# Optimization experiments

Measured on AMD Instinct MI355X. Metric: run time of the kernel, lower is better.

The kernel has to match this reference:

```python
import jax, jax.numpy as jnp
import numpy as np

B, T, I, H, L, O = 64, 1024, 256, 512, 2, 256


def setup_inputs() -> dict:
    key = jax.random.key(0)
    ks = jax.random.split(key, 12)
    s = 1.0 / np.sqrt(H)  # PyTorch RNN init scale
    return {
        "x": jax.random.normal(ks[0], (B, T, I), jnp.float32),
        "W_ih0": jax.random.normal(ks[1], (3 * H, I), jnp.float32) * s,
        "W_hh0": jax.random.normal(ks[2], (3 * H, H), jnp.float32) * s,
        "b_ih0": jax.random.normal(ks[3], (3 * H,), jnp.float32) * s,
        "b_hh0": jax.random.normal(ks[4], (3 * H,), jnp.float32) * s,
        "W_ih1": jax.random.normal(ks[5], (3 * H, H), jnp.float32) * s,
        "W_hh1": jax.random.normal(ks[6], (3 * H, H), jnp.float32) * s,
        "b_ih1": jax.random.normal(ks[7], (3 * H,), jnp.float32) * s,
        "b_hh1": jax.random.normal(ks[8], (3 * H,), jnp.float32) * s,
        "fc_w": jax.random.normal(ks[9], (O, H), jnp.float32) * s,
        "fc_b": jax.random.normal(ks[10], (O,), jnp.float32) * s,
    }


def gru_layer(x, W_ih, W_hh, b_ih, b_hh):
    """One PyTorch-convention GRU layer, batch_first input [B,T,*], h0=0."""
    Bt, Tt, _ = x.shape
    Hh = W_hh.shape[1]
    # Precompute input-side gate pre-activations for all timesteps: [T,B,3H]
    xg = (jnp.einsum('bti,gi->btg', x, W_ih) + b_ih).transpose(1, 0, 2)

    def step(h, xg_t):
        hg = h @ W_hh.T + b_hh                      # [B,3H]
        xr, xz, xn = jnp.split(xg_t, 3, axis=-1)
        hr, hz, hn = jnp.split(hg, 3, axis=-1)
        r = jax.nn.sigmoid(xr + hr)
        z = jax.nn.sigmoid(xz + hz)
        n = jnp.tanh(xn + r * hn)
        h_new = (1.0 - z) * n + z * h
        return h_new, h_new

    h0 = jnp.zeros((Bt, Hh), x.dtype)
    hT, hs = jax.lax.scan(step, h0, xg)
    return hs.transpose(1, 0, 2), hT  # [B,T,H], [B,H]


def reference(x, W_ih0, W_hh0, b_ih0, b_hh0, W_ih1, W_hh1, b_ih1, b_hh1, fc_w, fc_b):
    out0, h0 = gru_layer(x, W_ih0, W_hh0, b_ih0, b_hh0)
    out1, h1 = gru_layer(out0, W_ih1, W_hh1, b_ih1, b_hh1)
    hidden = jnp.stack([h0, h1], axis=0)            # [num_layers, B, H]
    flat = out1.reshape(-1, out1.shape[-1])          # [B*T, H]
    out = flat @ fc_w.T + fc_b                       # [B*T, O]
    return out, hidden
```

## Files before the change

kernel.cpp:

```cpp
#include <hip/hip_runtime.h>
#include <hip/hip_bf16.h>
#include <hip/hip_fp16.h>
#include <stdint.h>
#include <type_traits>

#define B_ 64
#define T_ 1024
#define I_ 256
#define H_ 512
#define G3_ 1536
#define O_ 256

typedef __attribute__((ext_vector_type(4))) float floatx4;
typedef __attribute__((ext_vector_type(8))) short short8;
typedef __attribute__((ext_vector_type(2))) _Float16 half2v;
typedef __attribute__((ext_vector_type(4))) unsigned int u32x4;

#define BARX() __asm__ volatile("s_waitcnt lgkmcnt(0)\n\ts_barrier" ::: "memory")

static __device__ __forceinline__ float fdot2f(uint32_t a, uint32_t b, float c) {
#if __has_builtin(__builtin_amdgcn_fdot2)
  return __builtin_amdgcn_fdot2(__builtin_bit_cast(half2v, a),
                                __builtin_bit_cast(half2v, b), c, false);
#else
  __half2 ha = __builtin_bit_cast(__half2, a);
  __half2 hb = __builtin_bit_cast(__half2, b);
  float2 fa = __half22float2(ha), fb = __half22float2(hb);
  return c + fa.x * fb.x + fa.y * fb.y;
#endif
}

static __device__ __forceinline__ float sigmoid_f(float x) {
  float e = __expf(-fabsf(x));
  float a = 1.f / (1.f + e);
  return x >= 0.f ? a : 1.f - a;
}
static __device__ __forceinline__ float tanh_f(float x) {
  float e = __expf(-2.f * fabsf(x));
  float a = (1.f - e) / (1.f + e);
  return x >= 0.f ? a : -a;
}
static __device__ __forceinline__ uint32_t pack_h2(float a, float b) {
  return (uint32_t)__half_as_ushort(__float2half(a)) |
         ((uint32_t)__half_as_ushort(__float2half(b)) << 16);
}
static __device__ __forceinline__ uint32_t pack_bf2(float a, float b) {
  return (uint32_t)__builtin_bit_cast(unsigned short, __float2bfloat16(a)) |
         ((uint32_t)__builtin_bit_cast(unsigned short, __float2bfloat16(b)) << 16);
}

__global__ void init_kernel(const float* __restrict__ Whh0, const float* __restrict__ Whh1,
                            const float* __restrict__ bih0, const float* __restrict__ bhh0,
                            const float* __restrict__ bih1, const float* __restrict__ bhh1,
                            uint32_t* __restrict__ wpack, float* __restrict__ biasv,
                            uint32_t* __restrict__ hstate) {
  int idx = blockIdx.x * 256 + threadIdx.x;
  if (idx < 786432) {
    int l = idx / 393216, rem = idx % 393216;
    int rc = rem / 49152;
    int rem2 = rem % 49152;
    int s = rem2 / 6144;
    int rem3 = rem2 % 6144;
    int j = rem3 / 96;
    int i = rem3 % 96;
    int g = i >> 5, pp = i & 31;
    const float* W = l ? Whh1 : Whh0;
    int row = g * 512 + rc * 64 + j;
    int k = s * 64 + pp * 2;
    uint32_t lo = __half_as_ushort(__float2half(W[(size_t)row * 512 + k]));
    uint32_t hi = __half_as_ushort(__float2half(W[(size_t)row * 512 + k + 1]));
    wpack[idx] = lo | (hi << 16);
  }
  int i2 = idx - 786432;
  if (i2 >= 0 && i2 < 3072) {
    int l = i2 / 1536, n = i2 % 1536;
    const float* bi = l ? bih1 : bih0;
    const float* bh = l ? bhh1 : bhh0;
    biasv[i2] = bi[n] + (n < 1024 ? bh[n] : 0.f);
  }
  int i3 = idx - (786432 + 3072);
  if (i3 >= 0 && i3 < 32768) hstate[i3] = 0u;
}

template <typename TA, typename TC>
__global__ __launch_bounds__(256, 2) void gemm_bt(
    const TA* __restrict__ A, const float* __restrict__ Bw,
    const float* __restrict__ bias, TC* __restrict__ C,
    int K, int lda, int ldc, int tcshift, int t0, int Ttot) {
  __shared__ unsigned short As[128 * 40];
  __shared__ unsigned short Bs[128 * 40];
  const int tid = threadIdx.x;
  const int bm = blockIdx.x, bn = blockIdx.y;
  const int r = tid >> 1, hf = tid & 1;

  const int m = bm * 128 + r;
  const long arow = (long)(m >> tcshift) * Ttot + t0 + (m & ((1 << tcshift) - 1));
  const TA* ap = A + arow * (long)lda + hf * 16;
  const int n = bn * 128 + r;
  const float* bp = Bw + (long)n * K + hf * 16;

  const int wid = tid >> 6, lane = tid & 63;
  const int wm = (wid >> 1) * 64, wn = (wid & 1) * 64;
  const int m16 = lane & 15, quad = lane >> 4;

  floatx4 acc[4][4];
#pragma unroll
  for (int i = 0; i < 4; ++i)
#pragma unroll
    for (int j = 0; j < 4; ++j) acc[i][j] = 0.f;

  for (int k0 = 0; k0 < K; k0 += 32) {
    unsigned short ta[16], tb[16];
    if constexpr (std::is_same<TA, float>::value) {
      const float4* p = (const float4*)(ap + k0);
#pragma unroll
      for (int q = 0; q < 4; ++q) {
        float4 v = p[q];
        ta[q * 4 + 0] = __builtin_bit_cast(unsigned short, __float2bfloat16(v.x));
        ta[q * 4 + 1] = __builtin_bit_cast(unsigned short, __float2bfloat16(v.y));
        ta[q * 4 + 2] = __builtin_bit_cast(unsigned short, __float2bfloat16(v.z));
        ta[q * 4 + 3] = __builtin_bit_cast(unsigned short, __float2bfloat16(v.w));
      }
    } else {
      const uint4* p = (const uint4*)(ap + k0);
      *(uint4*)&ta[0] = p[0];
      *(uint4*)&ta[8] = p[1];
    }
    {
      const float4* p = (const float4*)(bp + k0);
#pragma unroll
      for (int q = 0; q < 4; ++q) {
        float4 v = p[q];
        tb[q * 4 + 0] = __builtin_bit_cast(unsigned short, __float2bfloat16(v.x));
        tb[q * 4 + 1] = __builtin_bit_cast(unsigned short, __float2bfloat16(v.y));
        tb[q * 4 + 2] = __builtin_bit_cast(unsigned short, __float2bfloat16(v.z));
        tb[q * 4 + 3] = __builtin_bit_cast(unsigned short, __float2bfloat16(v.w));
      }
    }
    *(uint4*)&As[r * 40 + hf * 16] = *(uint4*)&ta[0];
    *(uint4*)&As[r * 40 + hf * 16 + 8] = *(uint4*)&ta[8];
    *(uint4*)&Bs[r * 40 + hf * 16] = *(uint4*)&tb[0];
    *(uint4*)&Bs[r * 40 + hf * 16 + 8] = *(uint4*)&tb[8];
    __syncthreads();
    short8 af[4], bfr[4];
#pragma unroll
    for (int mt = 0; mt < 4; ++mt)
      af[mt] = *(const short8*)&As[(wm + mt * 16 + m16) * 40 + quad * 8];
#pragma unroll
    for (int nt = 0; nt < 4; ++nt)
      bfr[nt] = *(const short8*)&Bs[(wn + nt * 16 + m16) * 40 + quad * 8];
#pragma unroll
    for (int mt = 0; mt < 4; ++mt)
#pragma unroll
      for (int nt = 0; nt < 4; ++nt)
        acc[mt][nt] = __builtin_amdgcn_mfma_f32_16x16x32_bf16(af[mt], bfr[nt],
                                                              acc[mt][nt], 0, 0, 0);
    __syncthreads();
  }
#pragma unroll
  for (int mt = 0; mt < 4; ++mt)
#pragma unroll
    for (int nt = 0; nt < 4; ++nt)
#pragma unroll
      for (int rr = 0; rr < 4; ++rr) {
        int grow = bm * 128 + wm + mt * 16 + quad * 4 + rr;
        int gcol = bn * 128 + wn + nt * 16 + m16;
        float v = acc[mt][nt][rr];
        if (bias) v += bias[gcol];
        if constexpr (std::is_same<TC, float>::value)
          C[(long)grow * ldc + gcol] = v;
        else
          C[(long)grow * ldc + gcol] = __float2half(v);
      }
}

__global__ __launch_bounds__(512, 1) void gru_rec(
    const uint32_t* __restrict__ wpack, const uint32_t* __restrict__ xgd,
    const float* __restrict__ bhh, uint32_t* __restrict__ hstate,
    uint32_t* __restrict__ outw, uint64_t* __restrict__ pkts,
    float* __restrict__ hid_out,
    int t0, int Tc, int outT, int outT0, int last) {
  const int tid = threadIdx.x;
  const int s = tid >> 6;
  const int j = tid & 63;
  const int bp = blockIdx.x & 31;
  const int rc = blockIdx.x >> 5;
  const int b2 = j >> 5;
  const int m = j & 31;
  const int bgat = 2 * bp + b2;

  __shared__ uint32_t hb[2][8][32];
  __shared__ float part[2][2][3][8][64];

  u32x4 W[24];
  {
    const uint32_t* wb = wpack + (((size_t)rc * 8 + s) * 64 + j) * 96;
#pragma unroll
    for (int q = 0; q < 24; ++q)
      asm volatile("global_load_dwordx4 %0, %1, off"
                   : "=v"(W[q])
                   : "v"(wb + q * 4));
    asm volatile("s_waitcnt vmcnt(0)" ::: "memory");
  }

  float hold0 = 0.f, hold1 = 0.f, bn0 = 0.f, bn1 = 0.f;
  uint32_t xrw = 0, xzw = 0, xnw = 0;
  if (s == 0) {
    uint32_t hv = hstate[bgat * 256 + rc * 32 + m];
    __half2 hh = __builtin_bit_cast(__half2, hv);
    hold0 = __half2float(hh.x);
    hold1 = __half2float(hh.y);
    bn0 = bhh[1024 + rc * 64 + 2 * m];
    bn1 = bhh[1024 + rc * 64 + 2 * m + 1];
    size_t base = ((size_t)bgat * Tc) * 768 + rc * 32 + m;
    xrw = xgd[base];
    xzw = xgd[base + 256];
    xnw = xgd[base + 512];
  }

  for (int tt = 0; tt < Tc; ++tt) {
    const int t = t0 + tt;
    uint32_t hp;
    if (tt == 0) {
      hp = hstate[bgat * 256 + s * 32 + m];
    } else {
      const uint64_t* pp = &pkts[(((size_t)(t & 1)) * 64 + bgat) * 256 + s * 32 + m];
      uint64_t v;
      do {
        v = __hip_atomic_load(pp, __ATOMIC_RELAXED, __HIP_MEMORY_SCOPE_AGENT);
      } while ((uint32_t)(v >> 32) != (uint32_t)t);
      hp = (uint32_t)v;
    }
    hb[b2][s][m] = hp;
    float ar0 = 0.f, az0 = 0.f, an0 = 0.f;
    float ar1 = 0.f, az1 = 0.f, an1 = 0.f;
#pragma unroll
    for (int p4 = 0; p4 < 8; ++p4) {
      uint4 u0 = *((const uint4*)&hb[0][s][0] + p4);
      uint4 u1 = *((const uint4*)&hb[1][s][0] + p4);
      u32x4 wr = W[p4], wz = W[8 + p4], wn = W[16 + p4];
      ar0 = fdot2f(wr[0], u0.x, ar0); az0 = fdot2f(wz[0], u0.x, az0); an0 = fdot2f(wn[0], u0.x, an0);
      ar0 = fdot2f(wr[1], u0.y, ar0); az0 = fdot2f(wz[1], u0.y, az0); an0 = fdot2f(wn[1], u0.y, an0);
      ar0 = fdot2f(wr[2], u0.z, ar0); az0 = fdot2f(wz[2], u0.z, az0); an0 = fdot2f(wn[2], u0.z, an0);
      ar0 = fdot2f(wr[3], u0.w, ar0); az0 = fdot2f(wz[3], u0.w, az0); an0 = fdot2f(wn[3], u0.w, an0);
      ar1 = fdot2f(wr[0], u1.x, ar1); az1 = fdot2f(wz[0], u1.x, az1); an1 = fdot2f(wn[0], u1.x, an1);
      ar1 = fdot2f(wr[1], u1.y, ar1); az1 = fdot2f(wz[1], u1.y, az1); an1 = fdot2f(wn[1], u1.y, an1);
      ar1 = fdot2f(wr[2], u1.z, ar1); az1 = fdot2f(wz[2], u1.z, az1); an1 = fdot2f(wn[2], u1.z, an1);
      ar1 = fdot2f(wr[3], u1.w, ar1); az1 = fdot2f(wz[3], u1.w, az1); an1 = fdot2f(wn[3], u1.w, an1);
    }
    const int ps = t & 1;
    part[ps][0][0][s][j] = ar0;
    part[ps][0][1][s][j] = az0;
    part[ps][0][2][s][j] = an0;
    part[ps][1][0][s][j] = ar1;
    part[ps][1][1][s][j] = az1;
    part[ps][1][2][s][j] = an1;
    BARX();

    if (s == 0) {
      float hr0 = 0.f, hr1 = 0.f, hz0 = 0.f, hz1 = 0.f, hn0 = 0.f, hn1 = 0.f;
#pragma unroll
      for (int ss = 0; ss < 8; ++ss) {
        float2 vr = *(const float2*)&part[ps][b2][0][ss][2 * m];
        float2 vz = *(const float2*)&part[ps][b2][1][ss][2 * m];
        float2 vn = *(const float2*)&part[ps][b2][2][ss][2 * m];
        hr0 += vr.x; hr1 += vr.y;
        hz0 += vz.x; hz1 += vz.y;
        hn0 += vn.x; hn1 += vn.y;
      }
      __half2 xr = __builtin_bit_cast(__half2, xrw);
      __half2 xz = __builtin_bit_cast(__half2, xzw);
      __half2 xn = __builtin_bit_cast(__half2, xnw);
      float r0 = sigmoid_f(__half2float(xr.x) + hr0);
      float r1 = sigmoid_f(__half2float(xr.y) + hr1);
      float z0 = sigmoid_f(__half2float(xz.x) + hz0);
      float z1 = sigmoid_f(__half2float(xz.y) + hz1);
      float n0 = tanh_f(__half2float(xn.x) + r0 * (hn0 + bn0));
      float n1 = tanh_f(__half2float(xn.y) + r1 * (hn1 + bn1));
      float h0 = (1.f - z0) * n0 + z0 * hold0;
      float h1 = (1.f - z1) * n1 + z1 * hold1;
      hold0 = h0;
      hold1 = h1;
      uint32_t hd = pack_h2(h0, h1);
      uint64_t pk = (uint64_t)hd | ((uint64_t)(uint32_t)(t + 1) << 32);
      __hip_atomic_store(&pkts[(((size_t)((t + 1) & 1)) * 64 + bgat) * 256 + rc * 32 + m],
                         pk, __ATOMIC_RELAXED, __HIP_MEMORY_SCOPE_AGENT);
      outw[((size_t)bgat * outT + outT0 + tt) * 256 + rc * 32 + m] = pack_bf2(h0, h1);
      if (tt + 1 < Tc) {
        size_t base = ((size_t)bgat * Tc + tt + 1) * 768 + rc * 32 + m;
        xrw = xgd[base];
        xzw = xgd[base + 256];
        xnw = xgd[base + 512];
      }
    }
  }

  if (s == 0) {
    hstate[bgat * 256 + rc * 32 + m] = pack_h2(hold0, hold1);
    if (last) {
      float2 hv = make_float2(hold0, hold1);
      *(float2*)&hid_out[bgat * 512 + (rc * 32 + m) * 2] = hv;
    }
  }
}

extern "C" void kernel_launch(void* const* d_in, const int* in_sizes, int n_in,
                              void* d_out, int out_size, void* d_ws, size_t ws_size,
                              hipStream_t stream) {
  const float* x = (const float*)d_in[0];
  const float* W_ih0 = (const float*)d_in[1];
  const float* W_hh0 = (const float*)d_in[2];
  const float* b_ih0 = (const float*)d_in[3];
  const float* b_hh0 = (const float*)d_in[4];
  const float* W_ih1 = (const float*)d_in[5];
  const float* W_hh1 = (const float*)d_in[6];
  const float* b_ih1 = (const float*)d_in[7];
  const float* b_hh1 = (const float*)d_in[8];
  const float* fc_w = (const float*)d_in[9];
  const float* fc_b = (const float*)d_in[10];
  float* out = (float*)d_out;

  char* p = (char*)d_ws;
  size_t off = 0;
  auto alloc = [&](size_t bytes) -> void* {
    void* r = p + off;
    off = (off + bytes + 255) & ~(size_t)255;
    return r;
  };
  uint32_t* wpack = (uint32_t*)alloc((size_t)786432 * 4);
  float* biasv = (float*)alloc((size_t)3072 * 4);
  uint32_t* hstate = (uint32_t*)alloc((size_t)32768 * 4);
  uint64_t* pkts = (uint64_t*)alloc((size_t)2 * 2 * 64 * 256 * 8);
  __hip_bfloat16* out1 = (__hip_bfloat16*)alloc((size_t)B_ * T_ * H_ * 2);

  int Tc = 1024;
  while (Tc > 64) {
    size_t need = (size_t)B_ * Tc * H_ * 2 + (size_t)B_ * Tc * G3_ * 2 + 1024;
    if (off + need <= ws_size) break;
    Tc >>= 1;
  }
  __hip_bfloat16* out0c = (__hip_bfloat16*)alloc((size_t)B_ * Tc * H_ * 2);
  __half* xg = (__half*)alloc((size_t)B_ * Tc * G3_ * 2);
  int tcs = __builtin_ctz(Tc);

  init_kernel<<<3212, 256, 0, stream>>>(W_hh0, W_hh1, b_ih0, b_hh0, b_ih1, b_hh1,
                                        wpack, biasv, hstate);

  for (int t0 = 0; t0 < 1024; t0 += Tc) {
    const int M = B_ * Tc;
    const int last = (t0 + Tc) == 1024;
    {
      dim3 gg(M / 128, G3_ / 128);
      gemm_bt<float, __half><<<gg, 256, 0, stream>>>(x, W_ih0, biasv, xg, I_, I_,
                                                     G3_, tcs, t0, 1024);
      gru_rec<<<256, 512, 0, stream>>>(wpack, (const uint32_t*)xg, b_hh0, hstate,
                                       (uint32_t*)out0c, pkts,
                                       out + 16777216, t0, Tc, Tc, 0, last);
    }
    {
      dim3 gg(M / 128, G3_ / 128);
      gemm_bt<__hip_bfloat16, __half><<<gg, 256, 0, stream>>>(
          out0c, W_ih1, biasv + 1536, xg, H_, H_, G3_, tcs, 0, Tc);
      gru_rec<<<256, 512, 0, stream>>>(wpack + 393216, (const uint32_t*)xg, b_hh1,
                                       hstate + 16384, (uint32_t*)out1,
                                       pkts + 32768,
                                       out + 16777216 + 32768, t0, Tc, 1024, t0, last);
    }
  }
  dim3 gf(65536 / 128, O_ / 128);
  gemm_bt<__hip_bfloat16, float><<<gf, 256, 0, stream>>>(out1, fc_w, fc_b, out,
                                                         H_, H_, O_, 10, 0, 1024);
}
```

Before: 4.719 ms.

## Split GRU recurrence to one batch per block and stream weights from memory

The recurrent kernel now gives each block a single batch row instead of a pair, doubling the grid to 512 blocks and allowing two blocks per CU. Weights are no longer held in registers across timesteps. They are reloaded from global memory (expected to hit cache) on every step, and each thread computes one output element rather than two. The goal is more parallelism and shorter per-step latency on the serial recurrence, at the cost of repeated weight loads and extra cross-block synchronisation traffic.

```diff
diff --git a/kernel.cpp b/kernel.cpp
--- a/kernel.cpp
+++ b/kernel.cpp
@@ -56,17 +56,16 @@
                             uint32_t* __restrict__ hstate) {
   int idx = blockIdx.x * 256 + threadIdx.x;
   if (idx < 786432) {
-    int l = idx / 393216, rem = idx % 393216;
-    int rc = rem / 49152;
-    int rem2 = rem % 49152;
-    int s = rem2 / 6144;
-    int rem3 = rem2 % 6144;
-    int j = rem3 / 96;
-    int i = rem3 % 96;
-    int g = i >> 5, pp = i & 31;
+    int l = idx / 393216, r = idx % 393216;
+    int i = r % 96;
+    int tb = r / 96;
+    int j = tb & 63;
+    int s = (tb >> 6) & 7;
+    int c = tb >> 9;
+    int g = i >> 5, dw = i & 31;
     const float* W = l ? Whh1 : Whh0;
-    int row = g * 512 + rc * 64 + j;
-    int k = s * 64 + pp * 2;
+    int row = g * 512 + c * 64 + j;
+    int k = (s * 32 + dw) * 2;
     uint32_t lo = __half_as_ushort(__float2half(W[(size_t)row * 512 + k]));
     uint32_t hi = __half_as_ushort(__float2half(W[(size_t)row * 512 + k + 1]));
     wpack[idx] = lo | (hi << 16);
@@ -174,7 +173,7 @@
       }
 }
 
-__global__ __launch_bounds__(512, 1) void gru_rec(
+__global__ __launch_bounds__(512, 2) void gru_rec(
     const uint32_t* __restrict__ wpack, const uint32_t* __restrict__ xgd,
     const float* __restrict__ bhh, uint32_t* __restrict__ hstate,
     uint32_t* __restrict__ outw, uint64_t* __restrict__ pkts,
@@ -183,36 +182,24 @@
   const int tid = threadIdx.x;
   const int s = tid >> 6;
   const int j = tid & 63;
-  const int bp = blockIdx.x & 31;
-  const int rc = blockIdx.x >> 5;
-  const int b2 = j >> 5;
-  const int m = j & 31;
-  const int bgat = 2 * bp + b2;
-
-  __shared__ uint32_t hb[2][8][32];
-  __shared__ float part[2][2][3][8][64];
-
-  u32x4 W[24];
-  {
-    const uint32_t* wb = wpack + (((size_t)rc * 8 + s) * 64 + j) * 96;
-#pragma unroll
-    for (int q = 0; q < 24; ++q)
-      asm volatile("global_load_dwordx4 %0, %1, off"
-                   : "=v"(W[q])
-                   : "v"(wb + q * 4));
-    asm volatile("s_waitcnt vmcnt(0)" ::: "memory");
-  }
-
-  float hold0 = 0.f, hold1 = 0.f, bn0 = 0.f, bn1 = 0.f;
+  const int c = blockIdx.x & 7;
+  const int b = blockIdx.x >> 3;
+  const int m32 = j & 31;
+  const int p = c * 32 + (j >> 1);
+
+  __shared__ uint32_t hbw[8][32];
+  __shared__ float part[2][3][64][9];
+
+  const uint32_t* wp = wpack + ((size_t)(c * 8 + s) * 64 + j) * 96;
+
+  float hold = 0.f, bnv = 0.f;
   uint32_t xrw = 0, xzw = 0, xnw = 0;
   if (s == 0) {
-    uint32_t hv = hstate[bgat * 256 + rc * 32 + m];
+    uint32_t hv = hstate[b * 256 + p];
     __half2 hh = __builtin_bit_cast(__half2, hv);
-    hold0 = __half2float(hh.x);
-    hold1 = __half2float(hh.y);
-    bn0 = bhh[1024 + rc * 64 + 2 * m];
-    bn1 = bhh[1024 + rc * 64 + 2 * m + 1];
-    size_t base = ((size_t)bgat * Tc) * 768 + rc * 32 + m;
+    hold = (j & 1) ? __half2float(hh.y) : __half2float(hh.x);
+    bnv = bhh[1024 + c * 64 + j];
+    size_t base = ((size_t)b * Tc) * 768 + p;
     xrw = xgd[base];
     xzw = xgd[base + 256];
     xnw = xgd[base + 512];
@@ -222,72 +209,63 @@
     const int t = t0 + tt;
     uint32_t hp;
     if (tt == 0) {
-      hp = hstate[bgat * 256 + s * 32 + m];
+      hp = hstate[b * 256 + s * 32 + m32];
     } else {
-      const uint64_t* pp = &pkts[(((size_t)(t & 1)) * 64 + bgat) * 256 + s * 32 + m];
+      const uint64_t* pp = &pkts[(((size_t)(t & 1)) * 64 + b) * 256 + s * 32 + m32];
       uint64_t v;
       do {
         v = __hip_atomic_load(pp, __ATOMIC_RELAXED, __HIP_MEMORY_SCOPE_AGENT);
       } while ((uint32_t)(v >> 32) != (uint32_t)t);
       hp = (uint32_t)v;
     }
-    hb[b2][s][m] = hp;
-    float ar0 = 0.f, az0 = 0.f, an0 = 0.f;
-    float ar1 = 0.f, az1 = 0.f, an1 = 0.f;
-#pragma unroll
-    for (int p4 = 0; p4 < 8; ++p4) {
-      uint4 u0 = *((const uint4*)&hb[0][s][0] + p4);
-      uint4 u1 = *((const uint4*)&hb[1][s][0] + p4);
-      u32x4 wr = W[p4], wz = W[8 + p4], wn = W[16 + p4];
-      ar0 = fdot2f(wr[0], u0.x, ar0); az0 = fdot2f(wz[0], u0.x, az0); an0 = fdot2f(wn[0], u0.x, an0);
-      ar0 = fdot2f(wr[1], u0.y, ar0); az0 = fdot2f(wz[1], u0.y, az0); an0 = fdot2f(wn[1], u0.y, an0);
-      ar0 = fdot2f(wr[2], u0.z, ar0); az0 = fdot2f(wz[2], u0.z, az0); an0 = fdot2f(wn[2], u0.z, an0);
-      ar0 = fdot2f(wr[3], u0.w, ar0); az0 = fdot2f(wz[3], u0.w, az0); an0 = fdot2f(wn[3], u0.w, an0);
-      ar1 = fdot2f(wr[0], u1.x, ar1); az1 = fdot2f(wz[0], u1.x, az1); an1 = fdot2f(wn[0], u1.x, an1);
-      ar1 = fdot2f(wr[1], u1.y, ar1); az1 = fdot2f(wz[1], u1.y, az1); an1 = fdot2f(wn[1], u1.y, an1);
-      ar1 = fdot2f(wr[2], u1.z, ar1); az1 = fdot2f(wz[2], u1.z, az1); an1 = fdot2f(wn[2], u1.z, an1);
-      ar1 = fdot2f(wr[3], u1.w, ar1); az1 = fdot2f(wz[3], u1.w, az1); an1 = fdot2f(wn[3], u1.w, an1);
+    hbw[s][m32] = hp;
+    float ar = 0.f, az = 0.f, an = 0.f;
+#pragma unroll
+    for (int d4 = 0; d4 < 8; ++d4) {
+      uint4 H = *((const uint4*)&hbw[s][0] + d4);
+      u32x4 wr = *(const u32x4*)(wp + d4 * 4);
+      u32x4 wz = *(const u32x4*)(wp + 32 + d4 * 4);
+      u32x4 wn = *(const u32x4*)(wp + 64 + d4 * 4);
+      ar = fdot2f(wr[0], H.x, ar); az = fdot2f(wz[0], H.x, az); an = fdot2f(wn[0], H.x, an);
+      ar = fdot2f(wr[1], H.y, ar); az = fdot2f(wz[1], H.y, az); an = fdot2f(wn[1], H.y, an);
+      ar = fdot2f(wr[2], H.z, ar); az = fdot2f(wz[2], H.z, az); an = fdot2f(wn[2], H.z, an);
+      ar = fdot2f(wr[3], H.w, ar); az = fdot2f(wz[3], H.w, az); an = fdot2f(wn[3], H.w, an);
     }
     const int ps = t & 1;
-    part[ps][0][0][s][j] = ar0;
-    part[ps][0][1][s][j] = az0;
-    part[ps][0][2][s][j] = an0;
-    part[ps][1][0][s][j] = ar1;
-    part[ps][1][1][s][j] = az1;
-    part[ps][1][2][s][j] = an1;
+    part[ps][0][j][s] = ar;
+    part[ps][1][j][s] = az;
+    part[ps][2][j][s] = an;
     BARX();
 
     if (s == 0) {
-      float hr0 = 0.f, hr1 = 0.f, hz0 = 0.f, hz1 = 0.f, hn0 = 0.f, hn1 = 0.f;
+      float hr = 0.f, hz = 0.f, hn = 0.f;
 #pragma unroll
       for (int ss = 0; ss < 8; ++ss) {
-        float2 vr = *(const float2*)&part[ps][b2][0][ss][2 * m];
-        float2 vz = *(const float2*)&part[ps][b2][1][ss][2 * m];
-        float2 vn = *(const float2*)&part[ps][b2][2][ss][2 * m];
-        hr0 += vr.x; hr1 += vr.y;
-        hz0 += vz.x; hz1 += vz.y;
-        hn0 += vn.x; hn1 += vn.y;
-      }
-      __half2 xr = __builtin_bit_cast(__half2, xrw);
-      __half2 xz = __builtin_bit_cast(__half2, xzw);
-      __half2 xn = __builtin_bit_cast(__half2, xnw);
-      float r0 = sigmoid_f(__half2float(xr.x) + hr0);
-      float r1 = sigmoid_f(__half2float(xr.y) + hr1);
-      float z0 = sigmoid_f(__half2float(xz.x) + hz0);
-      float z1 = sigmoid_f(__half2float(xz.y) + hz1);
-      float n0 = tanh_f(__half2float(xn.x) + r0 * (hn0 + bn0));
-      float n1 = tanh_f(__half2float(xn.y) + r1 * (hn1 + bn1));
-      float h0 = (1.f - z0) * n0 + z0 * hold0;
-      float h1 = (1.f - z1) * n1 + z1 * hold1;
-      hold0 = h0;
-      hold1 = h1;
-      uint32_t hd = pack_h2(h0, h1);
-      uint64_t pk = (uint64_t)hd | ((uint64_t)(uint32_t)(t + 1) << 32);
-      __hip_atomic_store(&pkts[(((size_t)((t + 1) & 1)) * 64 + bgat) * 256 + rc * 32 + m],
-                         pk, __ATOMIC_RELAXED, __HIP_MEMORY_SCOPE_AGENT);
-      outw[((size_t)bgat * outT + outT0 + tt) * 256 + rc * 32 + m] = pack_bf2(h0, h1);
+        hr += part[ps][0][j][ss];
+        hz += part[ps][1][j][ss];
+        hn += part[ps][2][j][ss];
+      }
+      __half2 xr2 = __builtin_bit_cast(__half2, xrw);
+      __half2 xz2 = __builtin_bit_cast(__half2, xzw);
+      __half2 xn2 = __builtin_bit_cast(__half2, xnw);
+      float xr = (j & 1) ? __half2float(xr2.y) : __half2float(xr2.x);
+      float xz = (j & 1) ? __half2float(xz2.y) : __half2float(xz2.x);
+      float xn = (j & 1) ? __half2float(xn2.y) : __half2float(xn2.x);
+      float r = sigmoid_f(xr + hr);
+      float z = sigmoid_f(xz + hz);
+      float n = tanh_f(xn + r * (hn + bnv));
+      float h = (1.f - z) * n + z * hold;
+      hold = h;
+      float hq = __shfl_down(h, 1);
+      if ((j & 1) == 0) {
+        uint32_t hd = pack_h2(h, hq);
+        uint64_t pk = (uint64_t)hd | ((uint64_t)(uint32_t)(t + 1) << 32);
+        __hip_atomic_store(&pkts[(((size_t)((t + 1) & 1)) * 64 + b) * 256 + p],
+                           pk, __ATOMIC_RELAXED, __HIP_MEMORY_SCOPE_AGENT);
+        outw[((size_t)b * outT + outT0 + tt) * 256 + p] = pack_bf2(h, hq);
+      }
       if (tt + 1 < Tc) {
-        size_t base = ((size_t)bgat * Tc + tt + 1) * 768 + rc * 32 + m;
+        size_t base = ((size_t)b * Tc + tt + 1) * 768 + p;
         xrw = xgd[base];
         xzw = xgd[base + 256];
         xnw = xgd[base + 512];
@@ -296,10 +274,13 @@
   }
 
   if (s == 0) {
-    hstate[bgat * 256 + rc * 32 + m] = pack_h2(hold0, hold1);
-    if (last) {
-      float2 hv = make_float2(hold0, hold1);
-      *(float2*)&hid_out[bgat * 512 + (rc * 32 + m) * 2] = hv;
+    float hq2 = __shfl_down(hold, 1);
+    if ((j & 1) == 0) {
+      hstate[b * 256 + p] = pack_h2(hold, hq2);
+      if (last) {
+        float2 hv = make_float2(hold, hq2);
+        *(float2*)&hid_out[b * 512 + 2 * p] = hv;
+      }
     }
   }
 }
@@ -353,7 +334,7 @@
       dim3 gg(M / 128, G3_ / 128);
       gemm_bt<float, __half><<<gg, 256, 0, stream>>>(x, W_ih0, biasv, xg, I_, I_,
                                                      G3_, tcs, t0, 1024);
-      gru_rec<<<256, 512, 0, stream>>>(wpack, (const uint32_t*)xg, b_hh0, hstate,
+      gru_rec<<<512, 512, 0, stream>>>(wpack, (const uint32_t*)xg, b_hh0, hstate,
                                        (uint32_t*)out0c, pkts,
                                        out + 16777216, t0, Tc, Tc, 0, last);
     }
@@ -361,7 +342,7 @@
       dim3 gg(M / 128, G3_ / 128);
       gemm_bt<__hip_bfloat16, __half><<<gg, 256, 0, stream>>>(
           out0c, W_ih1, biasv + 1536, xg, H_, H_, G3_, tcs, 0, Tc);
-      gru_rec<<<256, 512, 0, stream>>>(wpack + 393216, (const uint32_t*)xg, b_hh1,
+      gru_rec<<<512, 512, 0, stream>>>(wpack + 393216, (const uint32_t*)xg, b_hh1,
                                        hstate + 16384, (uint32_t*)out1,
                                        pkts + 32768,
                                        out + 16777216 + 32768, t0, Tc, 1024, t0, last);
```

Measured after the change: 7.082 ms. 1.5x slower.
